# Kernel optimization log

Hardware: AMD Instinct MI355X
Metric: run time of the kernel (lower is better)

The kernel has to match this reference:

```python
import jax, jax.numpy as jnp
import numpy as np

HEADS = 3


def layernorm(x, scale, bias):
    mu = x.mean(-1, keepdims=True)
    var = ((x - mu) ** 2).mean(-1, keepdims=True)
    return (x - mu) * jax.lax.rsqrt(var + 1e-5) * scale + bias


def setup_inputs() -> dict:
    key = jax.random.key(0)
    ks = jax.random.split(key, 16)
    B, C, H, W = 8, 64, 32, 32
    hid, out, L = 384, 128, 3
    f32 = jnp.float32
    rn = lambda i, shape, sc: jax.random.normal(ks[i], shape, f32) * sc
    inp = {
        "x": rn(0, (B, C, H, W), 1.0),
        "W_enc": rn(1, (C, hid), 1.0 / np.sqrt(C)),
        "b_enc": jnp.zeros((hid,), f32),
        "gcn_W": rn(2, (L, hid, hid), 1.0 / np.sqrt(hid)),
        "gcn_b": jnp.zeros((L, hid), f32),
        "Wq": rn(3, (L, hid, hid), 1.0 / np.sqrt(hid)),
        "bq": jnp.zeros((L, hid), f32),
        "Wk": rn(4, (L, hid, hid), 1.0 / np.sqrt(hid)),
        "bk": jnp.zeros((L, hid), f32),
        "Wv": rn(5, (L, hid, hid), 1.0 / np.sqrt(hid)),
        "bv": jnp.zeros((L, hid), f32),
        "Wo": rn(6, (L, hid, hid), 1.0 / np.sqrt(hid)),
        "bo": jnp.zeros((L, hid), f32),
        "ln_scale": jnp.ones((L, 3, hid), f32),
        "ln_bias": jnp.zeros((L, 3, hid), f32),
        "mlp_W1": rn(7, (L, hid, 2 * hid), 1.0 / np.sqrt(hid)),
        "mlp_b1": jnp.zeros((L, 2 * hid), f32),
        "mlp_W2": rn(8, (L, 2 * hid, hid), 1.0 / np.sqrt(2 * hid)),
        "mlp_b2": jnp.zeros((L, hid), f32),
        "lin1_W": rn(9, (hid, hid), 1.0 / np.sqrt(hid)),
        "lin1_b": jnp.zeros((hid,), f32),
        "lin2_W": rn(10, (hid, out), 1.0 / np.sqrt(hid)),
        "lin2_b": jnp.zeros((out,), f32),
        "k": 16,
    }
    return inp


def reference(x, W_enc, b_enc, gcn_W, gcn_b, Wq, bq, Wk, bk, Wv, bv, Wo, bo,
              ln_scale, ln_bias, mlp_W1, mlp_b1, mlp_W2, mlp_b2,
              lin1_W, lin1_b, lin2_W, lin2_b, k):
    B, C, H, W = x.shape
    N = H * W
    L = gcn_W.shape[0]

    # node encoder (RWSE expand_x modeled as linear projection of pixel features)
    feats = x.reshape(B, C, N).transpose(0, 2, 1)            # [B, N, C]
    h0 = feats @ W_enc + b_enc                               # [B, N, hid]

    # cosine-similarity graph + kNN hypergraph build
    nh = h0 / jnp.linalg.norm(h0, axis=-1, keepdims=True)
    sim = jnp.einsum('bnd,bmd->bnm', nh, nh)                 # [B, N, N]
    sim = sim - 2.0 * jnp.eye(N, dtype=sim.dtype)            # exclude self-matches
    _, knn_idx = jax.lax.top_k(sim, k)                       # [B, N, k] neighbor (src) ids
    dst = jnp.broadcast_to(jnp.arange(N)[:, None], (N, k)).reshape(-1)  # [N*k]

    def gps_per_graph(hb, src_idx):
        src = src_idx.reshape(-1)                            # [N*k]
        deg = jax.ops.segment_sum(jnp.ones((N * k,), hb.dtype), dst, N) + 1.0  # self-loops
        norm = jax.lax.rsqrt(deg[src] * deg[dst])            # GCN sym norm
        hcur = hb
        for l in range(L):
            # --- local GCN message passing ---
            xw = hcur @ gcn_W[l] + gcn_b[l]                  # [N, hid]
            agg = jax.ops.segment_sum(xw[src] * norm[:, None], dst, N)
            agg = agg + xw / deg[:, None]                    # self-loop term
            h_local = layernorm(hcur + agg, ln_scale[l, 0], ln_bias[l, 0])
            # --- global multihead attention ---
            q = (hcur @ Wq[l] + bq[l]).reshape(N, HEADS, -1)
            kk = (hcur @ Wk[l] + bk[l]).reshape(N, HEADS, -1)
            v = (hcur @ Wv[l] + bv[l]).reshape(N, HEADS, -1)
            dh = q.shape[-1]
            scores = jnp.einsum('nhd,mhd->hnm', q, kk) * (1.0 / np.sqrt(dh))
            attn = jax.nn.softmax(scores, axis=-1)
            o = jnp.einsum('hnm,mhd->nhd', attn, v).reshape(N, -1) @ Wo[l] + bo[l]
            h_attn = layernorm(hcur + o, ln_scale[l, 1], ln_bias[l, 1])
            # --- combine + FFN ---
            out = h_local + h_attn
            out = out + jax.nn.relu(out @ mlp_W1[l] + mlp_b1[l]) @ mlp_W2[l] + mlp_b2[l]
            hcur = layernorm(out, ln_scale[l, 2], ln_bias[l, 2])
        return hcur.mean(axis=0)                             # global mean pool -> [hid]

    pooled = jax.vmap(gps_per_graph)(h0, knn_idx)            # [B, hid]
    z = jax.nn.relu(pooled @ lin1_W + lin1_b)
    return z @ lin2_W + lin2_b                               # [B, out]
```

## Files before the change

### kernel.cpp

```cpp
#include <hip/hip_runtime.h>
#include <hip/hip_bf16.h>

#define B_    8
#define C_    64
#define N_    1024
#define HID   384
#define OUTD  128
#define L_    3
#define KNN   16
#define NHEADS 3
#define DH    128

typedef __attribute__((ext_vector_type(8))) short    s16x8;
typedef __attribute__((ext_vector_type(4))) float    f32x4;
typedef __attribute__((ext_vector_type(8))) unsigned short u16x8;
typedef __attribute__((ext_vector_type(4))) unsigned short u16x4;

__device__ __forceinline__ ushort f2b(float f) {
    uint x = __float_as_uint(f);
    return (ushort)((x + 0x7fff + ((x >> 16) & 1)) >> 16);
}
__device__ __forceinline__ float b2f(uint u) {
    return __uint_as_float(u << 16);
}

__global__ void k_encode(const float* __restrict__ x, const float* __restrict__ Wenc,
                         const float* __restrict__ benc, float* __restrict__ h,
                         ushort* __restrict__ hb,
                         ushort* __restrict__ nhh, ushort* __restrict__ nhl) {
    int bn = blockIdx.x;
    int b = bn >> 10;
    const float* xb = x + (long)b * C_ * N_ + (bn & 1023);
    int tid = threadIdx.x;
    __shared__ float red[128];
    float val[3];
    #pragma unroll
    for (int i = 0; i < 3; ++i) {
        int c0 = tid + i * 128;
        float acc = benc[c0];
        for (int c = 0; c < C_; ++c)
            acc += xb[c * N_] * Wenc[c * HID + c0];
        h[(long)bn * HID + c0] = acc;
        hb[(long)bn * HID + c0] = f2b(acc);
        val[i] = acc;
    }
    float ss = 0.f;
    #pragma unroll
    for (int i = 0; i < 3; ++i) ss += val[i] * val[i];
    red[tid] = ss; __syncthreads();
    for (int s = 64; s > 0; s >>= 1) { if (tid < s) red[tid] += red[tid+s]; __syncthreads(); }
    float inv = 1.0f / sqrtf(red[0]);
    #pragma unroll
    for (int i = 0; i < 3; ++i) {
        int c0 = tid + i * 128;
        float fv = val[i] * inv;
        ushort hu = f2b(fv);
        float lo = fv - b2f((uint)hu);
        nhh[(long)bn * HID + c0] = hu;
        nhl[(long)bn * HID + c0] = f2b(lo);
    }
}

__global__ __launch_bounds__(256) void k_sim(const ushort* __restrict__ nhh,
                                             const ushort* __restrict__ nhl,
                                             float* __restrict__ sim) {
    __shared__ ushort Ah[128][40], Alo[128][40], Bh[128][40], Blo[128][40];
    int bz = blockIdx.z;
    int bm = blockIdx.y * 128, bn = blockIdx.x * 128;
    const ushort* baseh = nhh + (long)bz * N_ * HID;
    const ushort* basel = nhl + (long)bz * N_ * HID;
    int tid = threadIdx.x;
    int w = tid >> 6, l = tid & 63;
    int wm = w >> 1, wn = w & 1;
    int sr = tid >> 2, skq = (tid & 3) * 8;
    f32x4 acc[4][4] = {};
    for (int k0 = 0; k0 < HID; k0 += 32) {
        *(u16x8*)&Ah [sr][skq]      = *(const u16x8*)&baseh[(long)(bm + sr) * HID + k0 + skq];
        *(u16x8*)&Ah [sr + 64][skq] = *(const u16x8*)&baseh[(long)(bm + sr + 64) * HID + k0 + skq];
        *(u16x8*)&Alo[sr][skq]      = *(const u16x8*)&basel[(long)(bm + sr) * HID + k0 + skq];
        *(u16x8*)&Alo[sr + 64][skq] = *(const u16x8*)&basel[(long)(bm + sr + 64) * HID + k0 + skq];
        *(u16x8*)&Bh [sr][skq]      = *(const u16x8*)&baseh[(long)(bn + sr) * HID + k0 + skq];
        *(u16x8*)&Bh [sr + 64][skq] = *(const u16x8*)&baseh[(long)(bn + sr + 64) * HID + k0 + skq];
        *(u16x8*)&Blo[sr][skq]      = *(const u16x8*)&basel[(long)(bn + sr) * HID + k0 + skq];
        *(u16x8*)&Blo[sr + 64][skq] = *(const u16x8*)&basel[(long)(bn + sr + 64) * HID + k0 + skq];
        __syncthreads();
        s16x8 ah[4], al[4], bh[4], bl[4];
        #pragma unroll
        for (int mi = 0; mi < 4; ++mi) {
            ah[mi] = *(const s16x8*)&Ah [wm * 64 + mi * 16 + (l & 15)][(l >> 4) * 8];
            al[mi] = *(const s16x8*)&Alo[wm * 64 + mi * 16 + (l & 15)][(l >> 4) * 8];
        }
        #pragma unroll
        for (int ni = 0; ni < 4; ++ni) {
            bh[ni] = *(const s16x8*)&Bh [wn * 64 + ni * 16 + (l & 15)][(l >> 4) * 8];
            bl[ni] = *(const s16x8*)&Blo[wn * 64 + ni * 16 + (l & 15)][(l >> 4) * 8];
        }
        #pragma unroll
        for (int mi = 0; mi < 4; ++mi)
            #pragma unroll
            for (int ni = 0; ni < 4; ++ni) {
                acc[mi][ni] = __builtin_amdgcn_mfma_f32_16x16x32_bf16(ah[mi], bh[ni], acc[mi][ni], 0, 0, 0);
                acc[mi][ni] = __builtin_amdgcn_mfma_f32_16x16x32_bf16(ah[mi], bl[ni], acc[mi][ni], 0, 0, 0);
                acc[mi][ni] = __builtin_amdgcn_mfma_f32_16x16x32_bf16(al[mi], bh[ni], acc[mi][ni], 0, 0, 0);
            }
        __syncthreads();
    }
    float* so = sim + (long)bz * N_ * N_;
    #pragma unroll
    for (int mi = 0; mi < 4; ++mi) {
        int row0 = bm + wm * 64 + mi * 16 + (l >> 4) * 4;
        #pragma unroll
        for (int ni = 0; ni < 4; ++ni) {
            int coln = bn + wn * 64 + ni * 16 + (l & 15);
            #pragma unroll
            for (int reg = 0; reg < 4; ++reg)
                so[(long)(row0 + reg) * N_ + coln] = acc[mi][ni][reg];
        }
    }
}

__global__ __launch_bounds__(256) void k_topk(const float* __restrict__ sim, int* __restrict__ knn) {
    int tid = threadIdx.x;
    int wave = tid >> 6, ll = tid & 63;
    int bn = blockIdx.x * 4 + wave;
    int b = bn >> 10, n = bn & 1023;
    const float* row = sim + (long)b * N_ * N_ + (long)n * N_;
    float v[16];
    #pragma unroll
    for (int j = 0; j < 16; ++j) {
        int m = ll + j * 64;
        v[j] = row[m] - (m == n ? 2.0f : 0.0f);
    }
    int* kout = knn + (long)bn * KNN;
    for (int it = 0; it < KNN; ++it) {
        float bv = v[0]; int bi = ll;
        #pragma unroll
        for (int j = 1; j < 16; ++j)
            if (v[j] > bv) { bv = v[j]; bi = ll + j * 64; }
        #pragma unroll
        for (int mask = 1; mask < 64; mask <<= 1) {
            float ov = __shfl_xor(bv, mask);
            int   oi = __shfl_xor(bi, mask);
            if (ov > bv || (ov == bv && oi < bi)) { bv = ov; bi = oi; }
        }
        if (ll == 0) kout[it] = bi;
        if ((bi & 63) == ll) v[bi >> 6] = -1e30f;
    }
}

__global__ void k_cast15(const float* __restrict__ g, const float* __restrict__ q,
                         const float* __restrict__ k, const float* __restrict__ v,
                         const float* __restrict__ o, ushort* __restrict__ out) {
    int z = blockIdx.z; int type = z / 3, l = z % 3;
    const float* in = (type == 0 ? g : type == 1 ? q : type == 2 ? k : type == 3 ? v : o)
                      + (long)l * HID * HID;
    int slot = (type == 0) ? l : (type == 4) ? 12 + l : 3 + l * 3 + (type - 1);
    ushort* op = out + (long)slot * HID * HID;
    __shared__ float t[32][33];
    int c0 = blockIdx.x * 32, r0 = blockIdx.y * 32;
    int tid = threadIdx.x; int i = tid & 31, j4 = tid >> 5;
    #pragma unroll
    for (int rr = 0; rr < 4; ++rr) {
        int r = j4 * 4 + rr;
        t[r][i] = in[(long)(r0 + r) * HID + c0 + i];
    }
    __syncthreads();
    #pragma unroll
    for (int rr = 0; rr < 4; ++rr) {
        int c = j4 * 4 + rr;
        op[(long)(c0 + c) * HID + r0 + i] = f2b(t[i][c]);
    }
}

__global__ void k_castT(const float* __restrict__ in_, ushort* __restrict__ out_,
                        int R, int C) {
    long mz = (long)blockIdx.z * R * C;
    const float* in = in_ + mz;
    ushort* op = out_ + mz;
    __shared__ float t[32][33];
    int c0 = blockIdx.x * 32, r0 = blockIdx.y * 32;
    int tid = threadIdx.x; int i = tid & 31, j4 = tid >> 5;
    #pragma unroll
    for (int rr = 0; rr < 4; ++rr) {
        int r = j4 * 4 + rr;
        t[r][i] = in[(long)(r0 + r) * C + c0 + i];
    }
    __syncthreads();
    #pragma unroll
    for (int rr = 0; rr < 4; ++rr) {
        int c = j4 * 4 + rr;
        op[(long)(c0 + c) * R + r0 + i] = f2b(t[i][c]);
    }
}

__global__ void k_biasqkv(const float* __restrict__ bq, const float* __restrict__ bk,
                          const float* __restrict__ bv, float* __restrict__ qkvb) {
    int l = blockIdx.x, t = threadIdx.x;
    qkvb[l * 1152 + t]       = bq[l * HID + t];
    qkvb[l * 1152 + 384 + t] = bk[l * HID + t];
    qkvb[l * 1152 + 768 + t] = bv[l * HID + t];
}

template<int OUTMODE, bool RELU>
__global__ __launch_bounds__(256) void k_mgemm(
        const ushort* __restrict__ A, const ushort* __restrict__ Wt,
        const float* __restrict__ bias, const float* __restrict__ resid,
        void* __restrict__ Cout, void* __restrict__ CoutT,
        int M, int N, int K, long ldcT) {
    __shared__ ushort Al[128][40];
    __shared__ ushort Bl[128][40];
    int bm = blockIdx.y * 128, bnn = blockIdx.x * 128;
    int tid = threadIdx.x;
    int w = tid >> 6, l = tid & 63;
    int wm = w >> 1, wn = w & 1;
    int sr = tid >> 2, skq = (tid & 3) * 8;
    f32x4 acc[4][4] = {};
    for (int k0 = 0; k0 < K; k0 += 32) {
        *(u16x8*)&Al[sr][skq]      = *(const u16x8*)&A [(long)(bm + sr) * K + k0 + skq];
        *(u16x8*)&Al[sr + 64][skq] = *(const u16x8*)&A [(long)(bm + sr + 64) * K + k0 + skq];
        *(u16x8*)&Bl[sr][skq]      = *(const u16x8*)&Wt[(long)(bnn + sr) * K + k0 + skq];
        *(u16x8*)&Bl[sr + 64][skq] = *(const u16x8*)&Wt[(long)(bnn + sr + 64) * K + k0 + skq];
        __syncthreads();
        s16x8 af[4], bf[4];
        #pragma unroll
        for (int mi = 0; mi < 4; ++mi)
            af[mi] = *(const s16x8*)&Al[wm * 64 + mi * 16 + (l & 15)][(l >> 4) * 8];
        #pragma unroll
        for (int ni = 0; ni < 4; ++ni)
            bf[ni] = *(const s16x8*)&Bl[wn * 64 + ni * 16 + (l & 15)][(l >> 4) * 8];
        #pragma unroll
        for (int mi = 0; mi < 4; ++mi)
            #pragma unroll
            for (int ni = 0; ni < 4; ++ni)
                acc[mi][ni] = __builtin_amdgcn_mfma_f32_16x16x32_bf16(af[mi], bf[ni], acc[mi][ni], 0, 0, 0);
        __syncthreads();
    }
    #pragma unroll
    for (int mi = 0; mi < 4; ++mi) {
        int row0 = bm + wm * 64 + mi * 16 + (l >> 4) * 4;
        #pragma unroll
        for (int ni = 0; ni < 4; ++ni) {
            int coln = bnn + wn * 64 + ni * 16 + (l & 15);
            float bv = bias[coln];
            if (OUTMODE == 2) {
                u16x4 pk;
                #pragma unroll
                for (int reg = 0; reg < 4; ++reg)
                    pk[reg] = f2b(acc[mi][ni][reg] + bv);
                *(u16x4*)((ushort*)Cout + (long)coln * ldcT + row0) = pk;
            } else if (OUTMODE == 3) {
                if (coln < 768) {
                    #pragma unroll
                    for (int reg = 0; reg < 4; ++reg)
                        ((ushort*)Cout)[(long)(row0 + reg) * 768 + coln] = f2b(acc[mi][ni][reg] + bv);
                } else {
                    u16x4 pk;
                    #pragma unroll
                    for (int reg = 0; reg < 4; ++reg)
                        pk[reg] = f2b(acc[mi][ni][reg] + bv);
                    *(u16x4*)((ushort*)CoutT + (long)(coln - 768) * ldcT + row0) = pk;
                }
            } else {
                #pragma unroll
                for (int reg = 0; reg < 4; ++reg) {
                    int rowg = row0 + reg;
                    float v = acc[mi][ni][reg] + bv;
                    if (resid) v += resid[(long)rowg * N + coln];
                    if (RELU)  v = fmaxf(v, 0.f);
                    if (OUTMODE == 0) ((float*)Cout)[(long)rowg * N + coln] = v;
                    else              ((ushort*)Cout)[(long)rowg * N + coln] = f2b(v);
                }
            }
        }
    }
}

__global__ void k_gcn_ln(const float* __restrict__ h, const float* __restrict__ xw,
                         const int* __restrict__ knn,
                         const float* __restrict__ lns, const float* __restrict__ lnb,
                         float* __restrict__ hlocal) {
    int bn = blockIdx.x; int b = bn >> 10;
    __shared__ int nb[KNN];
    __shared__ float red[128];
    int tid = threadIdx.x;
    if (tid < KNN) nb[tid] = knn[(long)bn * KNN + tid];
    __syncthreads();
    float val[3]; float sum = 0.f, ssq = 0.f;
    #pragma unroll
    for (int i = 0; i < 3; ++i) {
        int c = tid + i * 128;
        float acc = xw[(long)bn * HID + c];
        #pragma unroll
        for (int j = 0; j < KNN; ++j)
            acc += xw[((long)(b << 10) + nb[j]) * HID + c];
        float v = h[(long)bn * HID + c] + acc * (1.0f / 17.0f);
        val[i] = v; sum += v; ssq += v * v;
    }
    red[tid] = sum; __syncthreads();
    for (int s = 64; s > 0; s >>= 1) { if (tid < s) red[tid] += red[tid+s]; __syncthreads(); }
    sum = red[0]; __syncthreads();
    red[tid] = ssq; __syncthreads();
    for (int s = 64; s > 0; s >>= 1) { if (tid < s) red[tid] += red[tid+s]; __syncthreads(); }
    ssq = red[0];
    float mu = sum / HID;
    float var = ssq / HID - mu * mu;
    float inv = rsqrtf(var + 1e-5f);
    #pragma unroll
    for (int i = 0; i < 3; ++i) {
        int c = tid + i * 128;
        hlocal[(long)bn * HID + c] = (val[i] - mu) * inv * lns[c] + lnb[c];
    }
}

__global__ void k_addln(const float* __restrict__ a, const float* __restrict__ badd,
                        const float* __restrict__ post,
                        const float* __restrict__ lns, const float* __restrict__ lnb,
                        float* __restrict__ outp, ushort* __restrict__ bfout) {
    int bn = blockIdx.x;
    __shared__ float red[128];
    int tid = threadIdx.x;
    float val[3]; float sum = 0.f, ssq = 0.f;
    #pragma unroll
    for (int i = 0; i < 3; ++i) {
        int c = tid + i * 128;
        float v = a[(long)bn * HID + c];
        if (badd) v += badd[(long)bn * HID + c];
        val[i] = v; sum += v; ssq += v * v;
    }
    red[tid] = sum; __syncthreads();
    for (int s = 64; s > 0; s >>= 1) { if (tid < s) red[tid] += red[tid+s]; __syncthreads(); }
    sum = red[0]; __syncthreads();
    red[tid] = ssq; __syncthreads();
    for (int s = 64; s > 0; s >>= 1) { if (tid < s) red[tid] += red[tid+s]; __syncthreads(); }
    ssq = red[0];
    float mu = sum / HID;
    float var = ssq / HID - mu * mu;
    float inv = rsqrtf(var + 1e-5f);
    #pragma unroll
    for (int i = 0; i < 3; ++i) {
        int c = tid + i * 128;
        float o = (val[i] - mu) * inv * lns[c] + lnb[c];
        if (post) o += post[(long)bn * HID + c];
        outp[(long)bn * HID + c] = o;
        if (bfout) bfout[(long)bn * HID + c] = f2b(o);
    }
}

__global__ __launch_bounds__(256) void k_attn(const ushort* __restrict__ qk,
                                              const ushort* __restrict__ vt,
                                              ushort* __restrict__ o) {
    int b = blockIdx.z, hh = blockIdx.y, r0 = blockIdx.x * 16;
    __shared__ ushort sc[16][1032];
    __shared__ ushort kvt[9216];
    __shared__ float rowinv[16];
    int tid = threadIdx.x;
    int w = tid >> 6, l = tid & 63;
    s16x8 aq[4];
    const ushort* qrow = qk + ((long)(b * N_) + r0 + (l & 15)) * 768 + hh * DH + (l >> 4) * 8;
    #pragma unroll
    for (int ks = 0; ks < 4; ++ks) aq[ks] = *(const s16x8*)(qrow + ks * 32);
    const float scale = 0.08838834764831845f;
    for (int m0 = 0; m0 < N_; m0 += 64) {
        {
            int key = tid >> 2, seg = tid & 3;
            const ushort* src = qk + ((long)(b * N_) + m0 + key) * 768 + 384 + hh * DH + seg * 32;
            ushort* dst = &kvt[key * 136 + seg * 32];
            #pragma unroll
            for (int i = 0; i < 4; ++i)
                *(u16x8*)(dst + i * 8) = *(const u16x8*)(src + i * 8);
        }
        __syncthreads();
        f32x4 acc = {0.f, 0.f, 0.f, 0.f};
        #pragma unroll
        for (int ks = 0; ks < 4; ++ks) {
            s16x8 bk = *(const s16x8*)&kvt[(w * 16 + (l & 15)) * 136 + ks * 32 + (l >> 4) * 8];
            acc = __builtin_amdgcn_mfma_f32_16x16x32_bf16(aq[ks], bk, acc, 0, 0, 0);
        }
        int key = m0 + w * 16 + (l & 15);
        #pragma unroll
        for (int reg = 0; reg < 4; ++reg)
            sc[(l >> 4) * 4 + reg][key] = f2b(acc[reg] * scale);
        __syncthreads();
    }
    {
        int g = tid >> 5, l2 = tid & 31;
        #pragma unroll
        for (int rr = 0; rr < 2; ++rr) {
            int row = g + rr * 8;
            float v[32];
            #pragma unroll
            for (int i = 0; i < 16; ++i) {
                uint u = *(const uint*)&sc[row][l2 * 2 + i * 64];
                v[2*i]   = b2f(u & 0xffffu);
                v[2*i+1] = b2f(u >> 16);
            }
            float mx = v[0];
            #pragma unroll
            for (int i = 1; i < 32; ++i) mx = fmaxf(mx, v[i]);
            #pragma unroll
            for (int m = 16; m >= 1; m >>= 1) mx = fmaxf(mx, __shfl_xor(mx, m));
            float sm = 0.f;
            #pragma unroll
            for (int i = 0; i < 16; ++i) {
                float e0 = __expf(v[2*i]   - mx);
                float e1 = __expf(v[2*i+1] - mx);
                sm += e0 + e1;
                *(uint*)&sc[row][l2 * 2 + i * 64] = (uint)f2b(e0) | ((uint)f2b(e1) << 16);
            }
            #pragma unroll
            for (int m = 16; m >= 1; m >>= 1) sm += __shfl_xor(sm, m);
            if (l2 == 0) rowinv[row] = 1.0f / sm;
        }
    }
    __syncthreads();
    f32x4 zero = {0.f, 0.f, 0.f, 0.f};
    f32x4 oacc[2] = {zero, zero};
    for (int m0 = 0; m0 < N_; m0 += 64) {
        {
            int dim = tid >> 1, half = tid & 1;
            const ushort* src = vt + ((long)(hh * DH + dim)) * (B_ * N_) + b * N_ + m0 + half * 32;
            ushort* dst = &kvt[dim * 72 + half * 32];
            #pragma unroll
            for (int i = 0; i < 4; ++i)
                *(u16x8*)(dst + i * 8) = *(const u16x8*)(src + i * 8);
        }
        __syncthreads();
        #pragma unroll
        for (int ks = 0; ks < 2; ++ks) {
            s16x8 pf = *(const s16x8*)&sc[l & 15][m0 + ks * 32 + (l >> 4) * 8];
            #pragma unroll
            for (int d = 0; d < 2; ++d) {
                s16x8 vf = *(const s16x8*)&kvt[((w * 2 + d) * 16 + (l & 15)) * 72 + ks * 32 + (l >> 4) * 8];
                oacc[d] = __builtin_amdgcn_mfma_f32_16x16x32_bf16(pf, vf, oacc[d], 0, 0, 0);
            }
        }
        __syncthreads();
    }
    #pragma unroll
    for (int d = 0; d < 2; ++d) {
        int dim = (w * 2 + d) * 16 + (l & 15);
        #pragma unroll
        for (int reg = 0; reg < 4; ++reg) {
            int row = (l >> 4) * 4 + reg;
            o[((long)(b * N_) + r0 + row) * HID + hh * DH + dim] = f2b(oacc[d][reg] * rowinv[row]);
        }
    }
}

__global__ __launch_bounds__(384) void k_pool1(const float* __restrict__ h,
                                               float* __restrict__ partial) {
    int s = blockIdx.x, b = blockIdx.y;
    int c = threadIdx.x;
    const float* hp = h + ((long)(b * N_) + s * 32) * HID + c;
    float acc = 0.f;
    #pragma unroll
    for (int n = 0; n < 32; ++n) acc += hp[(long)n * HID];
    partial[((long)(b * 32) + s) * HID + c] = acc;
}
__global__ __launch_bounds__(384) void k_pool2(const float* __restrict__ partial,
                                               float* __restrict__ pooled) {
    int b = blockIdx.x;
    int c = threadIdx.x;
    const float* pp = partial + (long)(b * 32) * HID + c;
    float acc = 0.f;
    #pragma unroll
    for (int s = 0; s < 32; ++s) acc += pp[(long)s * HID];
    pooled[b * HID + c] = acc * (1.0f / N_);
}

__global__ void k_head(const float* __restrict__ pooled,
                       const float* __restrict__ w1, const float* __restrict__ b1,
                       const float* __restrict__ w2, const float* __restrict__ b2,
                       float* __restrict__ out) {
    int b = blockIdx.x; int tid = threadIdx.x;
    __shared__ float z[HID];
    float acc = b1[tid];
    for (int c = 0; c < HID; ++c) acc += pooled[b * HID + c] * w1[c * HID + tid];
    z[tid] = fmaxf(acc, 0.f);
    __syncthreads();
    if (tid < OUTD) {
        float a2 = b2[tid];
        for (int j = 0; j < HID; ++j) a2 += z[j] * w2[j * OUTD + tid];
        out[b * OUTD + tid] = a2;
    }
}

extern "C" void kernel_launch(void* const* d_in, const int* in_sizes, int n_in,
                              void* d_out, int out_size, void* d_ws, size_t ws_size,
                              hipStream_t stream) {
    const float* x       = (const float*)d_in[0];
    const float* W_enc   = (const float*)d_in[1];
    const float* b_enc   = (const float*)d_in[2];
    const float* gcn_W   = (const float*)d_in[3];
    const float* gcn_b   = (const float*)d_in[4];
    const float* Wq      = (const float*)d_in[5];
    const float* bq      = (const float*)d_in[6];
    const float* Wk      = (const float*)d_in[7];
    const float* bk      = (const float*)d_in[8];
    const float* Wv      = (const float*)d_in[9];
    const float* bv      = (const float*)d_in[10];
    const float* Wo      = (const float*)d_in[11];
    const float* bo      = (const float*)d_in[12];
    const float* ln_s    = (const float*)d_in[13];
    const float* ln_b    = (const float*)d_in[14];
    const float* mlp_W1  = (const float*)d_in[15];
    const float* mlp_b1  = (const float*)d_in[16];
    const float* mlp_W2  = (const float*)d_in[17];
    const float* mlp_b2  = (const float*)d_in[18];
    const float* lin1_W  = (const float*)d_in[19];
    const float* lin1_b  = (const float*)d_in[20];
    const float* lin2_W  = (const float*)d_in[21];
    const float* lin2_b  = (const float*)d_in[22];

    const long S = (long)B_ * N_ * HID;
    char* base = (char*)d_ws;
    float* h      = (float*)(base);
    float* tmp1   = (float*)(base + (size_t)S * 4);
    float* hlocal = (float*)(base + (size_t)S * 8);
    float* outb   = (float*)(base + (size_t)S * 12);
    char*  tzone  = base + (size_t)S * 16;
    float* proj   = (float*)(base + (size_t)S * 24);
    float*  sim = (float*)tzone;
    ushort* qkbf = (ushort*)tzone;
    ushort* vbT  = (ushort*)(tzone + (size_t)S * 4);
    ushort* outb_bf = (ushort*)(tzone + (size_t)S * 6);
    ushort* tb  = (ushort*)tzone;
    ushort* nhh = (ushort*)(base + (size_t)S * 4);
    ushort* nhl = (ushort*)(base + (size_t)S * 6);
    int*    knn    = (int*)(base + (size_t)S * 28);
    float*  pooled = (float*)(base + (size_t)S * 28 + 524288);
    ushort* wts    = (ushort*)(base + (size_t)S * 28 + 524288 + 16384);
    const long SQ = (long)HID * HID;
    ushort* w1T = wts + 15 * SQ;
    ushort* w2T = w1T + 3 * (long)HID * 2 * HID;
    ushort* hb  = (ushort*)(base + (size_t)S * 28 + 524288 + 16384 + 7962624);
    float* qkvb = (float*)(base + (size_t)S * 28 + 524288 + 16384 + 7962624 + (size_t)S * 2);
    float* partial = tmp1;
    ushort* obf = (ushort*)tmp1;

    k_cast15<<<dim3(12, 12, 15), 256, 0, stream>>>(gcn_W, Wq, Wk, Wv, Wo, wts);
    k_castT<<<dim3(24, 12, 3), 256, 0, stream>>>(mlp_W1, w1T, HID, 2 * HID);
    k_castT<<<dim3(12, 24, 3), 256, 0, stream>>>(mlp_W2, w2T, 2 * HID, HID);
    k_biasqkv<<<3, 384, 0, stream>>>(bq, bk, bv, qkvb);

    k_encode<<<B_ * N_, 128, 0, stream>>>(x, W_enc, b_enc, h, hb, nhh, nhl);
    k_sim<<<dim3(8, 8, 8), 256, 0, stream>>>(nhh, nhl, sim);
    k_topk<<<B_ * N_ / 4, 256, 0, stream>>>(sim, knn);

    const int M = B_ * N_;
    for (int l = 0; l < L_; ++l) {
        const ushort* gWt  = wts + (long)l * SQ;
        const ushort* qkvW = wts + (long)(3 + l * 3) * SQ;
        const ushort* woT  = wts + (long)(12 + l) * SQ;
        const ushort* w1Tl = w1T + (long)l * HID * 2 * HID;
        const ushort* w2Tl = w2T + (long)l * HID * 2 * HID;
        const float* gB  = gcn_b + (long)l * HID;
        const float* bol = bo + (long)l * HID;
        const float* b1l = mlp_b1 + (long)l * 2 * HID;
        const float* b2l = mlp_b2 + (long)l * HID;
        const float* ls0 = ln_s + (long)(l * 3 + 0) * HID; const float* lb0 = ln_b + (long)(l * 3 + 0) * HID;
        const float* ls1 = ln_s + (long)(l * 3 + 1) * HID; const float* lb1 = ln_b + (long)(l * 3 + 1) * HID;
        const float* ls2 = ln_s + (long)(l * 3 + 2) * HID; const float* lb2 = ln_b + (long)(l * 3 + 2) * HID;

        k_mgemm<0, false><<<dim3(HID / 128, M / 128), 256, 0, stream>>>(
            hb, gWt, gB, nullptr, tmp1, nullptr, M, HID, HID, 0);
        k_gcn_ln<<<B_ * N_, 128, 0, stream>>>(h, tmp1, knn, ls0, lb0, hlocal);
        k_mgemm<3, false><<<dim3(1152 / 128, M / 128), 256, 0, stream>>>(
            hb, qkvW, qkvb + l * 1152, nullptr, qkbf, vbT, M, 1152, HID, (long)M);
        k_attn<<<dim3(N_ / 16, NHEADS, B_), 256, 0, stream>>>(qkbf, vbT, obf);
        k_mgemm<0, false><<<dim3(HID / 128, M / 128), 256, 0, stream>>>(
            obf, woT, bol, nullptr, proj, nullptr, M, HID, HID, 0);
        k_addln<<<B_ * N_, 128, 0, stream>>>(h, proj, hlocal, ls1, lb1, outb, outb_bf);
        k_mgemm<1, true><<<dim3(2 * HID / 128, M / 128), 256, 0, stream>>>(
            outb_bf, w1Tl, b1l, nullptr, tb, nullptr, M, 2 * HID, HID, 0);
        k_mgemm<0, false><<<dim3(HID / 128, M / 128), 256, 0, stream>>>(
            tb, w2Tl, b2l, outb, tmp1, nullptr, M, HID, 2 * HID, 0);
        k_addln<<<B_ * N_, 128, 0, stream>>>(tmp1, nullptr, nullptr, ls2, lb2, h, hb);
    }

    k_pool1<<<dim3(32, B_), 384, 0, stream>>>(h, partial);
    k_pool2<<<B_, 384, 0, stream>>>(partial, pooled);
    k_head<<<B_, HID, 0, stream>>>(pooled, lin1_W, lin1_b, lin2_W, lin2_b,
                                   (float*)d_out);
}
```

Baseline: 875.0 us.

## Fuse GCN and QKV GEMMs and load attention K/V directly from global

Reorders the cast weight slots so the GCN weight and Q/K/V weights of each layer are contiguous, letting one 1536-wide GEMM produce the fp32 GCN projection plus bf16 Q/K and transposed V in a single launch that reads the hidden activations once. The attention kernel drops its shared-memory staging of K and V tiles and feeds MFMA operands straight from global memory, removing per-tile barriers and LDS traffic. The trade-off is less coalesced global loads in attention, which rely on cache hits instead of explicit reuse.

```diff
diff --git a/kernel.cpp b/kernel.cpp
--- a/kernel.cpp
+++ b/kernel.cpp
@@ -154,7 +154,7 @@
     int z = blockIdx.z; int type = z / 3, l = z % 3;
     const float* in = (type == 0 ? g : type == 1 ? q : type == 2 ? k : type == 3 ? v : o)
                       + (long)l * HID * HID;
-    int slot = (type == 0) ? l : (type == 4) ? 12 + l : 3 + l * 3 + (type - 1);
+    int slot = (type == 4) ? 12 + l : l * 4 + type;
     ushort* op = out + (long)slot * HID * HID;
     __shared__ float t[32][33];
     int c0 = blockIdx.x * 32, r0 = blockIdx.y * 32;
@@ -193,19 +193,21 @@
     }
 }
 
-__global__ void k_biasqkv(const float* __restrict__ bq, const float* __restrict__ bk,
-                          const float* __restrict__ bv, float* __restrict__ qkvb) {
+__global__ void k_biasgqkv(const float* __restrict__ gb, const float* __restrict__ bq,
+                           const float* __restrict__ bk, const float* __restrict__ bv,
+                           float* __restrict__ out) {
     int l = blockIdx.x, t = threadIdx.x;
-    qkvb[l * 1152 + t]       = bq[l * HID + t];
-    qkvb[l * 1152 + 384 + t] = bk[l * HID + t];
-    qkvb[l * 1152 + 768 + t] = bv[l * HID + t];
+    out[l * 1536 + t]        = gb[l * HID + t];
+    out[l * 1536 + 384 + t]  = bq[l * HID + t];
+    out[l * 1536 + 768 + t]  = bk[l * HID + t];
+    out[l * 1536 + 1152 + t] = bv[l * HID + t];
 }
 
 template<int OUTMODE, bool RELU>
 __global__ __launch_bounds__(256) void k_mgemm(
         const ushort* __restrict__ A, const ushort* __restrict__ Wt,
         const float* __restrict__ bias, const float* __restrict__ resid,
-        void* __restrict__ Cout, void* __restrict__ CoutT,
+        void* __restrict__ Cout, void* __restrict__ CoutT, void* __restrict__ CoutF,
         int M, int N, int K, long ldcT) {
     __shared__ ushort Al[128][40];
     __shared__ ushort Bl[128][40];
@@ -242,23 +244,21 @@
         for (int ni = 0; ni < 4; ++ni) {
             int coln = bnn + wn * 64 + ni * 16 + (l & 15);
             float bv = bias[coln];
-            if (OUTMODE == 2) {
-                u16x4 pk;
-                #pragma unroll
-                for (int reg = 0; reg < 4; ++reg)
-                    pk[reg] = f2b(acc[mi][ni][reg] + bv);
-                *(u16x4*)((ushort*)Cout + (long)coln * ldcT + row0) = pk;
-            } else if (OUTMODE == 3) {
-                if (coln < 768) {
+            if (OUTMODE == 5) {
+                if (coln < 384) {
                     #pragma unroll
                     for (int reg = 0; reg < 4; ++reg)
-                        ((ushort*)Cout)[(long)(row0 + reg) * 768 + coln] = f2b(acc[mi][ni][reg] + bv);
+                        ((float*)CoutF)[(long)(row0 + reg) * HID + coln] = acc[mi][ni][reg] + bv;
+                } else if (coln < 1152) {
+                    #pragma unroll
+                    for (int reg = 0; reg < 4; ++reg)
+                        ((ushort*)Cout)[(long)(row0 + reg) * 768 + (coln - 384)] = f2b(acc[mi][ni][reg] + bv);
                 } else {
                     u16x4 pk;
                     #pragma unroll
                     for (int reg = 0; reg < 4; ++reg)
                         pk[reg] = f2b(acc[mi][ni][reg] + bv);
-                    *(u16x4*)((ushort*)CoutT + (long)(coln - 768) * ldcT + row0) = pk;
+                    *(u16x4*)((ushort*)CoutT + (long)(coln - 1152) * ldcT + row0) = pk;
                 }
             } else {
                 #pragma unroll
@@ -351,7 +351,6 @@
                                               ushort* __restrict__ o) {
     int b = blockIdx.z, hh = blockIdx.y, r0 = blockIdx.x * 16;
     __shared__ ushort sc[16][1032];
-    __shared__ ushort kvt[9216];
     __shared__ float rowinv[16];
     int tid = threadIdx.x;
     int w = tid >> 6, l = tid & 63;
@@ -361,27 +360,17 @@
     for (int ks = 0; ks < 4; ++ks) aq[ks] = *(const s16x8*)(qrow + ks * 32);
     const float scale = 0.08838834764831845f;
     for (int m0 = 0; m0 < N_; m0 += 64) {
-        {
-            int key = tid >> 2, seg = tid & 3;
-            const ushort* src = qk + ((long)(b * N_) + m0 + key) * 768 + 384 + hh * DH + seg * 32;
-            ushort* dst = &kvt[key * 136 + seg * 32];
-            #pragma unroll
-            for (int i = 0; i < 4; ++i)
-                *(u16x8*)(dst + i * 8) = *(const u16x8*)(src + i * 8);
-        }
-        __syncthreads();
+        int key = m0 + w * 16 + (l & 15);
+        const ushort* krow = qk + ((long)(b * N_) + key) * 768 + 384 + hh * DH + (l >> 4) * 8;
         f32x4 acc = {0.f, 0.f, 0.f, 0.f};
         #pragma unroll
-        for (int ks = 0; ks < 4; ++ks) {
-            s16x8 bk = *(const s16x8*)&kvt[(w * 16 + (l & 15)) * 136 + ks * 32 + (l >> 4) * 8];
-            acc = __builtin_amdgcn_mfma_f32_16x16x32_bf16(aq[ks], bk, acc, 0, 0, 0);
-        }
-        int key = m0 + w * 16 + (l & 15);
+        for (int ks = 0; ks < 4; ++ks)
+            acc = __builtin_amdgcn_mfma_f32_16x16x32_bf16(aq[ks], *(const s16x8*)(krow + ks * 32), acc, 0, 0, 0);
         #pragma unroll
         for (int reg = 0; reg < 4; ++reg)
             sc[(l >> 4) * 4 + reg][key] = f2b(acc[reg] * scale);
-        __syncthreads();
-    }
+    }
+    __syncthreads();
     {
         int g = tid >> 5, l2 = tid & 31;
         #pragma unroll
@@ -416,25 +405,17 @@
     f32x4 zero = {0.f, 0.f, 0.f, 0.f};
     f32x4 oacc[2] = {zero, zero};
     for (int m0 = 0; m0 < N_; m0 += 64) {
-        {
-            int dim = tid >> 1, half = tid & 1;
-            const ushort* src = vt + ((long)(hh * DH + dim)) * (B_ * N_) + b * N_ + m0 + half * 32;
-            ushort* dst = &kvt[dim * 72 + half * 32];
-            #pragma unroll
-            for (int i = 0; i < 4; ++i)
-                *(u16x8*)(dst + i * 8) = *(const u16x8*)(src + i * 8);
-        }
-        __syncthreads();
         #pragma unroll
         for (int ks = 0; ks < 2; ++ks) {
             s16x8 pf = *(const s16x8*)&sc[l & 15][m0 + ks * 32 + (l >> 4) * 8];
             #pragma unroll
             for (int d = 0; d < 2; ++d) {
-                s16x8 vf = *(const s16x8*)&kvt[((w * 2 + d) * 16 + (l & 15)) * 72 + ks * 32 + (l >> 4) * 8];
-                oacc[d] = __builtin_amdgcn_mfma_f32_16x16x32_bf16(pf, vf, oacc[d], 0, 0, 0);
+                int dim = (w * 2 + d) * 16 + (l & 15);
+                const ushort* vrow = vt + ((long)(hh * DH + dim)) * (B_ * N_) + b * N_
+                                       + m0 + ks * 32 + (l >> 4) * 8;
+                oacc[d] = __builtin_amdgcn_mfma_f32_16x16x32_bf16(pf, *(const s16x8*)vrow, oacc[d], 0, 0, 0);
             }
         }
-        __syncthreads();
     }
     #pragma unroll
     for (int d = 0; d < 2; ++d) {
@@ -534,14 +515,14 @@
     ushort* w1T = wts + 15 * SQ;
     ushort* w2T = w1T + 3 * (long)HID * 2 * HID;
     ushort* hb  = (ushort*)(base + (size_t)S * 28 + 524288 + 16384 + 7962624);
-    float* qkvb = (float*)(base + (size_t)S * 28 + 524288 + 16384 + 7962624 + (size_t)S * 2);
+    float* gqkvb = (float*)(base + (size_t)S * 28 + 524288 + 16384 + 7962624 + (size_t)S * 2);
     float* partial = tmp1;
     ushort* obf = (ushort*)tmp1;
 
     k_cast15<<<dim3(12, 12, 15), 256, 0, stream>>>(gcn_W, Wq, Wk, Wv, Wo, wts);
     k_castT<<<dim3(24, 12, 3), 256, 0, stream>>>(mlp_W1, w1T, HID, 2 * HID);
     k_castT<<<dim3(12, 24, 3), 256, 0, stream>>>(mlp_W2, w2T, 2 * HID, HID);
-    k_biasqkv<<<3, 384, 0, stream>>>(bq, bk, bv, qkvb);
+    k_biasgqkv<<<3, 384, 0, stream>>>(gcn_b, bq, bk, bv, gqkvb);
 
     k_encode<<<B_ * N_, 128, 0, stream>>>(x, W_enc, b_enc, h, hb, nhh, nhl);
     k_sim<<<dim3(8, 8, 8), 256, 0, stream>>>(nhh, nhl, sim);
@@ -549,12 +530,10 @@
 
     const int M = B_ * N_;
     for (int l = 0; l < L_; ++l) {
-        const ushort* gWt  = wts + (long)l * SQ;
-        const ushort* qkvW = wts + (long)(3 + l * 3) * SQ;
-        const ushort* woT  = wts + (long)(12 + l) * SQ;
+        const ushort* gqkvW = wts + (long)(l * 4) * SQ;
+        const ushort* woT   = wts + (long)(12 + l) * SQ;
         const ushort* w1Tl = w1T + (long)l * HID * 2 * HID;
         const ushort* w2Tl = w2T + (long)l * HID * 2 * HID;
-        const float* gB  = gcn_b + (long)l * HID;
         const float* bol = bo + (long)l * HID;
         const float* b1l = mlp_b1 + (long)l * 2 * HID;
         const float* b2l = mlp_b2 + (long)l * HID;
@@ -562,19 +541,17 @@
         const float* ls1 = ln_s + (long)(l * 3 + 1) * HID; const float* lb1 = ln_b + (long)(l * 3 + 1) * HID;
         const float* ls2 = ln_s + (long)(l * 3 + 2) * HID; const float* lb2 = ln_b + (long)(l * 3 + 2) * HID;
 
-        k_mgemm<0, false><<<dim3(HID / 128, M / 128), 256, 0, stream>>>(
-            hb, gWt, gB, nullptr, tmp1, nullptr, M, HID, HID, 0);
+        k_mgemm<5, false><<<dim3(1536 / 128, M / 128), 256, 0, stream>>>(
+            hb, gqkvW, gqkvb + l * 1536, nullptr, qkbf, vbT, tmp1, M, 1536, HID, (long)M);
         k_gcn_ln<<<B_ * N_, 128, 0, stream>>>(h, tmp1, knn, ls0, lb0, hlocal);
-        k_mgemm<3, false><<<dim3(1152 / 128, M / 128), 256, 0, stream>>>(
-            hb, qkvW, qkvb + l * 1152, nullptr, qkbf, vbT, M, 1152, HID, (long)M);
         k_attn<<<dim3(N_ / 16, NHEADS, B_), 256, 0, stream>>>(qkbf, vbT, obf);
         k_mgemm<0, false><<<dim3(HID / 128, M / 128), 256, 0, stream>>>(
-            obf, woT, bol, nullptr, proj, nullptr, M, HID, HID, 0);
+            obf, woT, bol, nullptr, proj, nullptr, nullptr, M, HID, HID, 0);
         k_addln<<<B_ * N_, 128, 0, stream>>>(h, proj, hlocal, ls1, lb1, outb, outb_bf);
         k_mgemm<1, true><<<dim3(2 * HID / 128, M / 128), 256, 0, stream>>>(
-            outb_bf, w1Tl, b1l, nullptr, tb, nullptr, M, 2 * HID, HID, 0);
+            outb_bf, w1Tl, b1l, nullptr, tb, nullptr, nullptr, M, 2 * HID, HID, 0);
         k_mgemm<0, false><<<dim3(HID / 128, M / 128), 256, 0, stream>>>(
-            tb, w2Tl, b2l, outb, tmp1, nullptr, M, HID, 2 * HID, 0);
+            tb, w2Tl, b2l, outb, tmp1, nullptr, nullptr, M, HID, 2 * HID, 0);
         k_addln<<<B_ * N_, 128, 0, stream>>>(tmp1, nullptr, nullptr, ls2, lb2, h, hb);
     }
 
```

New measurement: 917.3 us. 4.8% more time.
